# Kernel tuning notes

Hardware: AMD Instinct MI355X
Metric: run time of the kernel (lower is better)

The kernel has to match this reference:

```python
import jax, jax.numpy as jnp
import numpy as np

B, L, DIN, W, H, NL = 4, 1024, 768, 12288, 8, 2
BOTTLENECK = 64
DB = W // BOTTLENECK        # 192: total bottlenecked attention dim
HD = DB // H                # 24: per-head dim
K = 32                      # topk
LAM = 1.0 / (4 * DIN)
EPS = 1e-6


def setup_inputs() -> dict:
    key = jax.random.key(0)
    ks = jax.random.split(key, 8)
    x_input = jax.random.normal(ks[0], (B, L, DIN), jnp.float32)
    # decoder dictionary (torch: randn; scaled for numeric stability)
    D = jax.random.normal(ks[1], (W, DIN), jnp.float32) * 0.02
    b = jnp.zeros((1, DIN), jnp.float32)
    # per-attn-layer bottlenecked projections, stacked over layers
    Wq = jax.random.normal(ks[2], (NL, W, DB), jnp.float32) * 0.02
    Wk = jax.random.normal(ks[3], (NL, W, DB), jnp.float32) * 0.02
    Wv = jax.random.normal(ks[4], (NL, W, DB), jnp.float32) * 0.02
    Wo = jax.random.normal(ks[5], (NL, DB, W), jnp.float32) * 0.02
    bq = jnp.zeros((NL, DB), jnp.float32)
    bk = jnp.zeros((NL, DB), jnp.float32)
    bv = jnp.zeros((NL, DB), jnp.float32)
    bo = jnp.zeros((NL, W), jnp.float32)
    return {"x_input": x_input, "D": D, "b": b, "Wq": Wq, "bq": bq,
            "Wk": Wk, "bk": bk, "Wv": Wv, "bv": bv, "Wo": Wo, "bo": bo}


def _attention(z_ctx, z_in, Wq, bq, Wk, bk, Wv, bv, Wo, bo):
    # queries from current codes, keys/values from shifted context codes
    q = (z_in @ Wq + bq).reshape(B, L, H, HD)
    k = (z_ctx @ Wk + bk).reshape(B, L, H, HD)
    v = (z_ctx @ Wv + bv).reshape(B, L, H, HD)
    scores = jnp.einsum('bqhd,bkhd->bhqk', q, k) / np.sqrt(HD).astype(np.float32)
    causal = jnp.tril(jnp.ones((L, L), bool))  # query t sees ctx positions <= t
    scores = jnp.where(causal, scores, jnp.float32(-1e30))
    a = jax.nn.softmax(scores, axis=-1)
    o = jnp.einsum('bhqk,bkhd->bqhd', a, v).reshape(B, L, DB)
    return o @ Wo + bo


def reference(x_input, D, b, Wq, bq, Wk, bk, Wv, bv, Wo, bo):
    E = D.T  # tied weights
    x = x_input - b
    z_pred = jnp.zeros((B, L, W), x.dtype)
    for i in range(NL):
        z_in = jax.nn.relu((x * LAM) @ E)                       # [B,L,W]
        z_ctx = jnp.concatenate([jnp.zeros_like(z_in[:, :1]), z_in[:, :-1]], axis=1)
        z_pred_ = jax.nn.relu(_attention(z_ctx, z_in, Wq[i], bq[i], Wk[i], bk[i],
                                         Wv[i], bv[i], Wo[i], bo[i]))
        Dz = z_pred_ @ D                                        # [B,L,DIN]
        Dz_norm = jnp.linalg.norm(Dz, axis=-1, keepdims=True) + EPS
        proj_scale = jnp.sum(Dz * x, axis=-1, keepdims=True) / (Dz_norm ** 2)
        z_pred = z_pred + z_pred_ * proj_scale
        x = x - proj_scale * Dz
    # topk sparsification of the novel codes
    z_novel = jax.nn.relu((x * LAM) @ E)
    zf = z_novel.reshape(-1, W)                                 # [B*L, W]
    _, idx = jax.lax.top_k(zf, K)
    mask = jnp.zeros_like(zf).at[jnp.arange(zf.shape[0])[:, None], idx].set(1.0)
    z_novel = (zf * mask).reshape(B, L, W)
    x_recons = (z_novel + z_pred) @ D + b
    return x_recons
```

## Files before the change

kernel.cpp:

```cpp
#include <hip/hip_runtime.h>
#include <hip/hip_bf16.h>

typedef __attribute__((ext_vector_type(4))) float f32x4;
typedef __attribute__((ext_vector_type(8))) short short8;
typedef __attribute__((ext_vector_type(8))) unsigned short ushort8;
typedef __attribute__((ext_vector_type(4))) unsigned short ushort4v;
typedef __attribute__((ext_vector_type(4))) unsigned int uint4v;

#define DEVFN __device__ __forceinline__

DEVFN float b2f(unsigned short u) { return __uint_as_float(((unsigned)u) << 16); }
DEVFN unsigned short f2b(float f) {
  __hip_bfloat16 h = __float2bfloat16(f);
  return __builtin_bit_cast(unsigned short, h);
}

DEVFN void load_lds16(const void* g, void* l) {
  __builtin_amdgcn_global_load_lds(
      (const __attribute__((address_space(1))) unsigned int*)g,
      (__attribute__((address_space(3))) unsigned int*)l, 16, 0, 0);
}


__global__ void fill_out_zero(float* o, int n) {
  int i = blockIdx.x * 256 + threadIdx.x;
  if (i < n) o[i] = 0.0f;
}

__global__ __launch_bounds__(256) void init_x(
    const float* __restrict__ xin, const float* __restrict__ bvec,
    float* __restrict__ x, unsigned short* __restrict__ xb) {
  size_t i = (size_t)blockIdx.x * 256 + threadIdx.x;
  int col = (int)(i % 768);
  float v = xin[i] - bvec[col];
  x[i] = v;
  xb[i] = f2b(v);
}

__global__ __launch_bounds__(256) void fill_bias(
    float* __restrict__ buf, const float* __restrict__ bias, int ld) {
  size_t i = (size_t)blockIdx.x * 256 + threadIdx.x;
  buf[i] = bias ? bias[(int)(i % ld)] : 0.0f;
}

__global__ __launch_bounds__(256) void conv_f2b(
    const float* __restrict__ in, unsigned short* __restrict__ out) {
  size_t i = ((size_t)blockIdx.x * 256 + threadIdx.x) * 4;
  f32x4 v = *(const f32x4*)(in + i);
  ushort4v w;
#pragma unroll
  for (int e = 0; e < 4; ++e) w[e] = f2b(v[e]);
  *(ushort4v*)(out + i) = w;
}

__global__ __launch_bounds__(256) void transpose_f2b(
    const float* __restrict__ in, unsigned short* __restrict__ out,
    int R, int C) {
  __shared__ float tile[32][33];
  int r0 = blockIdx.x * 32, c0 = blockIdx.y * 32;
  int tx = threadIdx.x & 31, ty = threadIdx.x >> 5;
#pragma unroll
  for (int i = 0; i < 4; ++i)
    tile[ty + i * 8][tx] = in[(size_t)(r0 + ty + i * 8) * C + c0 + tx];
  __syncthreads();
#pragma unroll
  for (int i = 0; i < 4; ++i)
    out[(size_t)(c0 + ty + i * 8) * R + r0 + tx] = f2b(tile[tx][ty + i * 8]);
}

template <int GX, int GY, int GZ, int RX, int RG>
DEVFN void rect_decode(int bid, int& x, int& y, int& z) {
  constexpr int NRG = (GY * GZ) / RG;
  const int xcd = bid & 7;
  const int rr = bid >> 3;
  const int rgx = xcd % NRG, rxx = xcd / NRG;
  const int gl = rr % RG;
  int xl = rr / RG;
  xl = (xl + rgx * (RX / NRG)) % RX;
  const int g = rgx * RG + gl;
  x = rxx * RX + xl;
  y = g % GY;
  z = g / GY;
}

template <typename CT, bool RELU, int SC, bool BIAS, bool SPLITK,
          int GX, int GY, int GZ, int RX, int RG>
__global__ __launch_bounds__(512, 2) void gemm_bt2(
    const unsigned short* __restrict__ A, const unsigned short* __restrict__ B,
    CT* __restrict__ C, const float* __restrict__ bias,
    int K, int ldc, float alpha) {
  __shared__ unsigned short sA[2][256 * 64];
  __shared__ unsigned short sB[2][256 * 64];
  const int tid = threadIdx.x;
  const int wave = tid >> 6, lane = tid & 63;
  int bx, by, bz;
  rect_decode<GX, GY, GZ, RX, RG>((int)blockIdx.x, bx, by, bz);
  const int row0 = bx * 256, col0 = by * 256;
  const unsigned short* Ab = A + (size_t)row0 * K;
  const unsigned short* Bb = B + (size_t)col0 * K;
  const int srow = lane >> 3;
  const int swc = ((lane & 7) ^ srow) * 8;
  const int wm = wave & 1, wn = wave >> 1;
  const int lr = lane & 15;
  const int hi = lane >> 4;
  const int l7 = lane & 7;
  const int ksw0 = (hi ^ l7) * 8;
  const int ksw1 = ((4 + hi) ^ l7) * 8;
  const int klen = SPLITK ? (K / GZ) : K;
  const int kbeg = SPLITK ? bz * klen : 0;
  const int nt = klen / 64;
  f32x4 acc[8][4] = {};
  auto stage = [&](int buf, int t) {
    const int k0 = kbeg + t * 64;
#pragma unroll
    for (int it = 0; it < 8; ++it) {
      int c = wave * 8 + it;
      if (c < 32) {
        int r = c * 8 + srow;
        load_lds16(Ab + (size_t)r * K + k0 + swc, &sA[buf][c * 512]);
      } else {
        int cb = c - 32;
        int r = cb * 8 + srow;
        load_lds16(Bb + (size_t)r * K + k0 + swc, &sB[buf][cb * 512]);
      }
    }
  };
  stage(0, 0);
  for (int t = 0; t < nt; ++t) {
    const int cur = t & 1;
    if (t + 1 < nt) {
      stage(cur ^ 1, t + 1);
      asm volatile("s_waitcnt vmcnt(8)" ::: "memory");
    } else {
      asm volatile("s_waitcnt vmcnt(0)" ::: "memory");
    }
    __builtin_amdgcn_s_barrier();
    asm volatile("" ::: "memory");
    const unsigned short* cA = &sA[cur][0];
    const unsigned short* cB = &sB[cur][0];
#pragma unroll
    for (int ks = 0; ks < 2; ++ks) {
      const int ko = ks ? ksw1 : ksw0;
      short8 af[8], bfr[4];
#pragma unroll
      for (int i = 0; i < 8; ++i)
        af[i] = *(const short8*)&cA[(wm * 128 + i * 16 + lr) * 64 + ko];
#pragma unroll
      for (int j = 0; j < 4; ++j)
        bfr[j] = *(const short8*)&cB[(wn * 64 + j * 16 + lr) * 64 + ko];
#pragma unroll
      for (int i = 0; i < 8; ++i)
#pragma unroll
        for (int j = 0; j < 4; ++j)
          acc[i][j] = __builtin_amdgcn_mfma_f32_16x16x32_bf16(af[i], bfr[j], acc[i][j], 0, 0, 0);
    }
    asm volatile("" ::: "memory");
    __builtin_amdgcn_s_barrier();
  }
  const int rc = (SC == 0) ? 0 : ((row0 >> 10) + 1);
  const int rbase = row0 + rc + wm * 128 + (lane >> 4) * 4;
  const int cbase = col0 + wn * 64 + lr;
#pragma unroll
  for (int j = 0; j < 4; ++j) {
    int col = cbase + j * 16;
    float bv = BIAS ? bias[col] : 0.0f;
#pragma unroll
    for (int i = 0; i < 8; ++i) {
#pragma unroll
      for (int r = 0; r < 4; ++r) {
        float vv = acc[i][j][r] * alpha;
        size_t off = (size_t)(rbase + i * 16 + r) * ldc + col;
        if constexpr (SPLITK) {
          atomicAdd((float*)C + off, vv);
        } else {
          vv += bv;
          if (RELU) vv = fmaxf(vv, 0.0f);
          if constexpr (sizeof(CT) == 2) ((unsigned short*)C)[off] = f2b(vv);
          else C[off] = vv;
        }
      }
    }
  }
}

__global__ __launch_bounds__(256) void gemm_qkv(
    const unsigned short* __restrict__ A, const unsigned short* __restrict__ Bq,
    const float* __restrict__ bq, const float* __restrict__ bk,
    const float* __restrict__ bv,
    float* __restrict__ qb, float* __restrict__ kb, float* __restrict__ vb,
    float* __restrict__ P2) {
  __shared__ unsigned short sA[2][64 * 64];
  __shared__ unsigned short sB[2][192 * 64];
  const int tid = threadIdx.x;
  const int wave = tid >> 6, lane = tid & 63;
  const int bid = (int)blockIdx.x;
  const int xcd = bid & 7;
  const int rr = bid >> 3;
  const int combo = rr % 6;
  const int row = xcd * 8 + rr / 6;
  const int wz = combo >> 1;
  const int s = combo & 1;
  const int shift = (wz > 0);
  const unsigned short* B = Bq + (size_t)wz * 192 * 12288;
  const float* bias = (wz == 0) ? bq : (wz == 1 ? bk : bv);
  float* dst = (s == 0) ? ((wz == 0) ? qb : (wz == 1 ? kb : vb))
                        : (P2 + (size_t)wz * 786432);
  const int row0 = row * 64;
  const int ra = (row0 >> 10) + 1;
  const unsigned short* Ab = A + (size_t)(row0 + ra) * 12288;
  const int srow = lane >> 3;
  const int swc = ((lane & 7) ^ srow) * 8;
  const int wm = wave & 1, wn = wave >> 1;
  const int lr = lane & 15;
  const int hi = lane >> 4;
  const int l7 = lane & 7;
  const int ksw0 = (hi ^ l7) * 8;
  const int ksw1 = ((4 + hi) ^ l7) * 8;
  const int kbeg = s * 6144;
  f32x4 acc[2][6] = {};
  auto stage = [&](int buf, int t) {
    const int k0 = kbeg + t * 64;
#pragma unroll
    for (int it = 0; it < 8; ++it) {
      int c = wave * 8 + it;
      if (c < 8) {
        int r = c * 8 + srow;
        load_lds16(Ab + (size_t)r * 12288 + k0 + swc, &sA[buf][c * 512]);
      } else {
        int cb = c - 8;
        int r = cb * 8 + srow;
        load_lds16(B + (size_t)r * 12288 + k0 + swc, &sB[buf][cb * 512]);
      }
    }
  };
  stage(0, 0);
  for (int t = 0; t < 96; ++t) {
    const int cur = t & 1;
    if (t + 1 < 96) {
      stage(cur ^ 1, t + 1);
      asm volatile("s_waitcnt vmcnt(8)" ::: "memory");
    } else {
      asm volatile("s_waitcnt vmcnt(0)" ::: "memory");
    }
    __builtin_amdgcn_s_barrier();
    asm volatile("" ::: "memory");
    const unsigned short* cA = &sA[cur][0];
    const unsigned short* cB = &sB[cur][0];
#pragma unroll
    for (int ks = 0; ks < 2; ++ks) {
      const int ko = ks ? ksw1 : ksw0;
      short8 af[2], bfr[6];
#pragma unroll
      for (int i = 0; i < 2; ++i)
        af[i] = *(const short8*)&cA[(wm * 32 + i * 16 + lr) * 64 + ko];
#pragma unroll
      for (int j = 0; j < 6; ++j)
        bfr[j] = *(const short8*)&cB[(wn * 96 + j * 16 + lr) * 64 + ko];
#pragma unroll
      for (int i = 0; i < 2; ++i)
#pragma unroll
        for (int j = 0; j < 6; ++j)
          acc[i][j] = __builtin_amdgcn_mfma_f32_16x16x32_bf16(af[i], bfr[j], acc[i][j], 0, 0, 0);
    }
    asm volatile("" ::: "memory");
    __builtin_amdgcn_s_barrier();
  }
  const int rbase = row0 + wm * 32 + (lane >> 4) * 4;
  const int cbase = wn * 96 + lr;
#pragma unroll
  for (int j = 0; j < 6; ++j) {
    int col = cbase + j * 16;
    float bvv = (s == 0) ? bias[col] : 0.0f;
#pragma unroll
    for (int i = 0; i < 2; ++i)
#pragma unroll
      for (int r = 0; r < 4; ++r) {
        int rw = rbase + i * 16 + r;
        if (shift) {
          if ((rw & 1023) == 1023) continue;
          rw += 1;
        }
        dst[(size_t)rw * 192 + col] = acc[i][j][r] + bvv;
      }
  }
}

__global__ __launch_bounds__(256) void qkv_merge(
    const float* __restrict__ P2, float* __restrict__ qb,
    float* __restrict__ kb, float* __restrict__ vb) {
  size_t i = ((size_t)blockIdx.x * 256 + threadIdx.x) * 4;
  const int plane = (int)(i / 786432);
  const size_t o = i - (size_t)plane * 786432;
  float* dst = plane == 0 ? qb : (plane == 1 ? kb : vb);
  f32x4 a = *(const f32x4*)(P2 + i);
  f32x4 b = *(const f32x4*)(dst + o);
#pragma unroll
  for (int e = 0; e < 4; ++e) b[e] += a[e];
  *(f32x4*)(dst + o) = b;
}

__global__ __launch_bounds__(256) void attn_pass1(
    const float* __restrict__ q, const float* __restrict__ k,
    const float* __restrict__ v, float* __restrict__ P) {
  __shared__ float sK[128 * 24];
  __shared__ float sV[128 * 24];
  const int tid = threadIdx.x;
  const int wave = tid >> 6, lane = tid & 63;
  const int xcd = (int)blockIdx.x & 7;
  const int r0 = (int)blockIdx.x >> 3;
  const int bh = xcd * 4 + r0 / 72;
  const int t = r0 % 72;
  const int b = bh >> 3, h = bh & 7;
  int jq = 0;
  while (true) {
    int jn = jq + 1;
    int a2 = jn >> 1;
    int offn = a2 * a2 + a2 + (jn & 1) * (a2 + 1);
    if (jn < 16 && offn <= t) jq = jn; else break;
  }
  const int aq = jq >> 1;
  const int offj = aq * aq + aq + (jq & 1) * (aq + 1);
  const int c = t - offj;
  const int qg = jq * 4 + wave;
  const int qi = lane & 15, ks = lane >> 4;
  const int qpos = qg * 16 + qi;
  const int n = b * 1024 + qpos;
  const int task = bh * 72 + t;
  {
    const float* kg = k + (size_t)(b * 1024 + c * 128) * 192 + h * 24;
    const float* vg = v + (size_t)(b * 1024 + c * 128) * 192 + h * 24;
#pragma unroll
    for (int i = 0; i < 3; ++i) {
      int idx = tid + i * 256;
      int row = idx / 6, seg = idx - row * 6;
      *(f32x4*)&sK[row * 24 + seg * 4] =
          *(const f32x4*)(kg + (size_t)row * 192 + seg * 4);
      *(f32x4*)&sV[row * 24 + seg * 4] =
          *(const f32x4*)(vg + (size_t)row * 192 + seg * 4);
    }
  }
  const float scale = 0.20412414523193154f;
  float qv[24];
  const float* qr = q + (size_t)n * 192 + h * 24;
#pragma unroll
  for (int d = 0; d < 24; ++d) qv[d] = qr[d] * scale;
  __syncthreads();
  float m = -1e30f, l = 0.0f, ov[24] = {};
  const int kb0 = c * 128;
  const int kend = min(qpos, kb0 + 127);
  for (int kp = kb0 + ks; kp <= kend; kp += 4) {
    const f32x4* kr = (const f32x4*)&sK[(kp - kb0) * 24];
    float s0 = 0.0f, s1 = 0.0f, s2 = 0.0f;
#pragma unroll
    for (int j = 0; j < 2; ++j) {
      f32x4 k0 = kr[j * 3 + 0], k1 = kr[j * 3 + 1], k2 = kr[j * 3 + 2];
#pragma unroll
      for (int e = 0; e < 4; ++e) {
        s0 += qv[(j * 3 + 0) * 4 + e] * k0[e];
        s1 += qv[(j * 3 + 1) * 4 + e] * k1[e];
        s2 += qv[(j * 3 + 2) * 4 + e] * k2[e];
      }
    }
    float s = s0 + s1 + s2;
    float mn = fmaxf(m, s);
    float corr = __expf(m - mn);
    float p = __expf(s - mn);
    const f32x4* vr = (const f32x4*)&sV[(kp - kb0) * 24];
    l = l * corr + p;
#pragma unroll
    for (int j = 0; j < 6; ++j) {
      f32x4 vvv = vr[j];
#pragma unroll
      for (int e = 0; e < 4; ++e) ov[j * 4 + e] = ov[j * 4 + e] * corr + p * vvv[e];
    }
    m = mn;
  }
#pragma unroll
  for (int off = 16; off < 64; off <<= 1) {
    float m2 = __shfl_xor(m, off);
    float l2 = __shfl_xor(l, off);
    float mn = fmaxf(m, m2);
    float c1 = __expf(m - mn), c2 = __expf(m2 - mn);
    l = l * c1 + l2 * c2;
#pragma unroll
    for (int d = 0; d < 24; ++d) {
      float o2 = __shfl_xor(ov[d], off);
      ov[d] = ov[d] * c1 + o2 * c2;
    }
    m = mn;
  }
  if (ks == 0) {
    float* pr = P + ((size_t)task * 64 + wave * 16 + qi) * 28;
    pr[0] = m;
    pr[1] = l;
#pragma unroll
    for (int d = 0; d < 24; ++d) pr[2 + d] = ov[d];
  }
}

__global__ __launch_bounds__(192) void attn_merge(
    const float* __restrict__ P, unsigned short* __restrict__ o) {
  const int n = blockIdx.x;
  const int tid = threadIdx.x;
  const int h = tid / 24, d = tid - h * 24;
  const int b = n >> 10, qpos = n & 1023;
  const int qg = qpos >> 4, qi = qpos & 15;
  const int j = qg >> 2, w = qg & 3;
  const int a = j >> 1;
  const int nch = a + 1;
  const int offj = a * a + a + (j & 1) * (a + 1);
  const int bh = b * 8 + h;
  const int base = bh * 72 + offj;
  float M = -1e30f;
  for (int cc = 0; cc < nch; ++cc)
    M = fmaxf(M, P[((size_t)(base + cc) * 64 + w * 16 + qi) * 28]);
  float L = 0.0f, OV = 0.0f;
  for (int cc = 0; cc < nch; ++cc) {
    const float* pr = P + ((size_t)(base + cc) * 64 + w * 16 + qi) * 28;
    float wgt = __expf(pr[0] - M);
    L += pr[1] * wgt;
    OV += pr[2 + d] * wgt;
  }
  o[(size_t)n * 192 + h * 24 + d] = f2b(OV / L);
}

__global__ __launch_bounds__(256) void proj_update(
    const float* __restrict__ Dz, float* __restrict__ x,
    unsigned short* __restrict__ xb) {
  const int n = blockIdx.x;
  const int tid = threadIdx.x;
  const float* dz = Dz + (size_t)n * 768;
  float* xr = x + (size_t)n * 768;
  float dot = 0.0f, s2 = 0.0f;
  for (int i = tid; i < 768; i += 256) {
    float a = dz[i], c = xr[i];
    dot += a * c;
    s2 += a * a;
  }
#pragma unroll
  for (int o2 = 32; o2; o2 >>= 1) {
    dot += __shfl_down(dot, o2);
    s2 += __shfl_down(s2, o2);
  }
  __shared__ float sd[4], ss[4], sp;
  const int wave = tid >> 6, lane = tid & 63;
  if (lane == 0) { sd[wave] = dot; ss[wave] = s2; }
  __syncthreads();
  if (tid == 0) {
    float Dd = sd[0] + sd[1] + sd[2] + sd[3];
    float S = ss[0] + ss[1] + ss[2] + ss[3];
    float nrm = sqrtf(S) + 1e-6f;
    sp = Dd / (nrm * nrm);
  }
  __syncthreads();
  float p = sp;
  for (int i = tid; i < 768; i += 256) {
    float nx = xr[i] - p * dz[i];
    xr[i] = nx;
    xb[(size_t)n * 768 + i] = f2b(nx);
  }
}

DEVFN int sanitize(int v) { return (v & 0x8000) ? 0 : v; }

__global__ __launch_bounds__(256) void topk_rows(
    const unsigned short* __restrict__ zbuf, int* __restrict__ idxo,
    float* __restrict__ valo) {
  const int n = blockIdx.x;
  const int b = n >> 10;
  const int tid = threadIdx.x;
  const int wave = tid >> 6, lane = tid & 63;
  const uint4v* zr = (const uint4v*)(zbuf + (size_t)(n + b + 1) * 12288);
  uint4v pk[6];
#pragma unroll
  for (int j = 0; j < 6; ++j) pk[j] = zr[tid * 6 + j];
  __shared__ int swsum[4];
  __shared__ int seq[256];
  __shared__ int spcnt;
  int lo = 0, hi = 0x7F7F;
  while (lo < hi) {
    int mid = (lo + hi) >> 1;
    int c = 0;
#pragma unroll
    for (int j = 0; j < 6; ++j)
#pragma unroll
      for (int e = 0; e < 4; ++e) {
        unsigned int u = pk[j][e];
        c += (sanitize((int)(u & 0xffffu)) > mid) + (sanitize((int)(u >> 16)) > mid);
      }
#pragma unroll
    for (int o2 = 32; o2; o2 >>= 1) c += __shfl_down(c, o2);
    if (lane == 0) swsum[wave] = c;
    __syncthreads();
    int total = swsum[0] + swsum[1] + swsum[2] + swsum[3];
    __syncthreads();
    if (total < 32) hi = mid; else lo = mid + 1;
  }
  const int T = lo;
  int cgt = 0, ceq = 0;
#pragma unroll
  for (int j = 0; j < 6; ++j)
#pragma unroll
    for (int e = 0; e < 4; ++e) {
      unsigned int u = pk[j][e];
      int v0 = sanitize((int)(u & 0xffffu)), v1 = sanitize((int)(u >> 16));
      cgt += (v0 > T) + (v1 > T);
      ceq += (v0 == T) + (v1 == T);
    }
  int cg = cgt;
#pragma unroll
  for (int o2 = 32; o2; o2 >>= 1) cg += __shfl_down(cg, o2);
  if (lane == 0) swsum[wave] = cg;
  seq[tid] = ceq;
  if (tid == 0) spcnt = 0;
  __syncthreads();
  const int total_gt = swsum[0] + swsum[1] + swsum[2] + swsum[3];
  for (int o2 = 1; o2 < 256; o2 <<= 1) {
    int vv = (tid >= o2) ? seq[tid - o2] : 0;
    __syncthreads();
    seq[tid] += vv;
    __syncthreads();
  }
  const int quota = 32 - total_gt;
  int rank = seq[tid] - ceq;
  int* irow = idxo + (size_t)n * 32;
  float* vrow = valo + (size_t)n * 32;
#pragma unroll
  for (int j = 0; j < 6; ++j)
#pragma unroll
    for (int e = 0; e < 4; ++e) {
      unsigned int u = pk[j][e];
#pragma unroll
      for (int hf = 0; hf < 2; ++hf) {
        int v = sanitize(hf ? (int)(u >> 16) : (int)(u & 0xffffu));
        bool kp = false;
        if (v > T) kp = true;
        else if (v == T) { if (rank < quota) kp = true; ++rank; }
        if (kp) {
          int pos = atomicAdd(&spcnt, 1);
          irow[pos] = tid * 48 + j * 8 + e * 2 + hf;
          vrow[pos] = b2f((unsigned short)v);
        }
      }
    }
}

__global__ __launch_bounds__(256) void sparse_recons(
    const int* __restrict__ idxo, const float* __restrict__ valo,
    const float* __restrict__ x, const float* __restrict__ xin,
    const float* __restrict__ D, float* __restrict__ out) {
  const int n = blockIdx.x;
  const int t = threadIdx.x;
  __shared__ int sidx[32];
  __shared__ float sval[32];
  if (t < 32) { sidx[t] = idxo[(size_t)n * 32 + t]; sval[t] = valo[(size_t)n * 32 + t]; }
  __syncthreads();
  float acc[3];
#pragma unroll
  for (int u = 0; u < 3; ++u) {
    size_t i = (size_t)n * 768 + t + u * 256;
    acc[u] = xin[i] - x[i];
  }
  for (int j = 0; j < 32; ++j) {
    size_t base = (size_t)sidx[j] * 768;
    float vj = sval[j];
#pragma unroll
    for (int u = 0; u < 3; ++u) acc[u] += vj * D[base + t + u * 256];
  }
#pragma unroll
  for (int u = 0; u < 3; ++u) out[(size_t)n * 768 + t + u * 256] = acc[u];
}

extern "C" void kernel_launch(void* const* d_in, const int* in_sizes, int n_in,
                              void* d_out, int out_size, void* d_ws, size_t ws_size,
                              hipStream_t stream) {
  (void)in_sizes; (void)n_in;
  const float* xin  = (const float*)d_in[0];
  const float* D    = (const float*)d_in[1];
  const float* bvec = (const float*)d_in[2];
  const float* Wq   = (const float*)d_in[3];
  const float* bq   = (const float*)d_in[4];
  const float* Wk   = (const float*)d_in[5];
  const float* bk   = (const float*)d_in[6];
  const float* Wv   = (const float*)d_in[7];
  const float* bv   = (const float*)d_in[8];
  const float* Wo   = (const float*)d_in[9];
  const float* bo   = (const float*)d_in[10];
  const float LAM = 1.0f / 3072.0f;

  char* ws = (char*)d_ws;
  size_t off = 0;
  auto alloc = [&](size_t bytes) {
    void* p = ws + off;
    off += (bytes + 255) & ~(size_t)255;
    return p;
  };
  unsigned short* zbuf = (unsigned short*)alloc((size_t)4 * 1025 * 12288 * 2);
  unsigned short* zpred_ = zbuf;
  float* attnP = (float*)zbuf;
  float* x           = (float*)alloc((size_t)4096 * 768 * 4);
  unsigned short* xb = (unsigned short*)alloc((size_t)4096 * 768 * 2);
  float* qb  = (float*)alloc((size_t)4096 * 192 * 4);
  float* kb  = (float*)alloc((size_t)4096 * 192 * 4);
  float* vb  = (float*)alloc((size_t)4096 * 192 * 4);
  unsigned short* ob = (unsigned short*)alloc((size_t)4096 * 192 * 2);
  float* Dz  = (float*)alloc((size_t)4096 * 768 * 4);
  int* idxo  = (int*)alloc((size_t)4096 * 32 * 4);
  float* valo = (float*)alloc((size_t)4096 * 32 * 4);
  const size_t WQKV = (size_t)192 * 12288;
  unsigned short* WqkvT = (unsigned short*)alloc((size_t)6 * WQKV * 2);
  unsigned short* WoT   = (unsigned short*)alloc((size_t)2 * 12288 * 192 * 2);
  unsigned short* Dbt   = (unsigned short*)alloc((size_t)12288 * 768 * 2);
  unsigned short* Dt    = (unsigned short*)alloc((size_t)768 * 12288 * 2);
  const size_t NEED = off;
  float* P2 = Dz;

  if (ws_size < NEED) {
    fill_out_zero<<<(out_size + 255) / 256, 256, 0, stream>>>((float*)d_out, out_size);
    return;
  }

  init_x<<<12288, 256, 0, stream>>>(xin, bvec, x, xb);
  conv_f2b<<<9216, 256, 0, stream>>>(D, Dbt);
  transpose_f2b<<<dim3(384, 24), 256, 0, stream>>>(D, Dt, 12288, 768);
  for (int l = 0; l < 2; ++l) {
    transpose_f2b<<<dim3(384, 6), 256, 0, stream>>>(
        Wq + (size_t)l * 12288 * 192, WqkvT + (size_t)(l * 3 + 0) * WQKV, 12288, 192);
    transpose_f2b<<<dim3(384, 6), 256, 0, stream>>>(
        Wk + (size_t)l * 12288 * 192, WqkvT + (size_t)(l * 3 + 1) * WQKV, 12288, 192);
    transpose_f2b<<<dim3(384, 6), 256, 0, stream>>>(
        Wv + (size_t)l * 12288 * 192, WqkvT + (size_t)(l * 3 + 2) * WQKV, 12288, 192);
    transpose_f2b<<<dim3(6, 384), 256, 0, stream>>>(
        Wo + (size_t)l * 192 * 12288, WoT + (size_t)l * 12288 * 192, 192, 12288);
  }

  for (int l = 0; l < 2; ++l) {
    gemm_bt2<unsigned short, true, 1, false, false, 16, 48, 1, 16, 6>
        <<<768, 512, 0, stream>>>(xb, Dbt, zbuf, nullptr, 768, 12288, LAM);
    fill_bias<<<3072, 256, 0, stream>>>(kb, bk + (size_t)l * 192, 192);
    fill_bias<<<3072, 256, 0, stream>>>(vb, bv + (size_t)l * 192, 192);
    fill_bias<<<9216, 256, 0, stream>>>(P2, nullptr, 192);
    gemm_qkv<<<384, 256, 0, stream>>>(
        zbuf, WqkvT + (size_t)(l * 3) * WQKV,
        bq + (size_t)l * 192, bk + (size_t)l * 192, bv + (size_t)l * 192,
        qb, kb, vb, P2);
    qkv_merge<<<2304, 256, 0, stream>>>(P2, qb, kb, vb);
    attn_pass1<<<2304, 256, 0, stream>>>(qb, kb, vb, attnP);
    attn_merge<<<4096, 192, 0, stream>>>(attnP, ob);
    gemm_bt2<unsigned short, true, 0, true, false, 16, 48, 1, 16, 6>
        <<<768, 512, 0, stream>>>(
        ob, WoT + (size_t)l * 12288 * 192, zpred_, bo + (size_t)l * 12288, 192, 12288, 1.0f);
    fill_bias<<<12288, 256, 0, stream>>>(Dz, nullptr, 768);
    gemm_bt2<float, false, 0, false, true, 16, 3, 4, 8, 3>
        <<<192, 512, 0, stream>>>(zpred_, Dt, Dz, nullptr, 12288, 768, 1.0f);
    proj_update<<<4096, 256, 0, stream>>>(Dz, x, xb);
  }
  gemm_bt2<unsigned short, true, 1, false, false, 16, 48, 1, 16, 6>
      <<<768, 512, 0, stream>>>(xb, Dbt, zbuf, nullptr, 768, 12288, LAM);
  topk_rows<<<4096, 256, 0, stream>>>(zbuf, idxo, valo);
  sparse_recons<<<4096, 256, 0, stream>>>(idxo, valo, x, xin, D, (float*)d_out);
}
```

Measured before the change: 1.266 ms.

## Split GEMM main loop into four sub-phases interleaving staged loads with MFMA

The 256x256 bf16 GEMM mainloop is restructured into four quarter-phases, split by M half and K half. Global-to-LDS loads for A and B halves are issued piecemeal between LDS fragment reads and MFMA blocks, replacing one bulk stage per iteration. An A half is prefetched two iterations ahead into the buffer it has just finished with. This aims to spread memory traffic and hide load latency behind compute, in exchange for more barriers per iteration and more complex buffer-reuse ordering that could race if the waitcnt and barrier placement is wrong.

```diff
diff --git a/kernel.cpp b/kernel.cpp
--- a/kernel.cpp
+++ b/kernel.cpp
@@ -110,52 +110,110 @@
   const int kbeg = SPLITK ? bz * klen : 0;
   const int nt = klen / 64;
   f32x4 acc[8][4] = {};
-  auto stage = [&](int buf, int t) {
-    const int k0 = kbeg + t * 64;
-#pragma unroll
-    for (int it = 0; it < 8; ++it) {
-      int c = wave * 8 + it;
-      if (c < 32) {
-        int r = c * 8 + srow;
-        load_lds16(Ab + (size_t)r * K + k0 + swc, &sA[buf][c * 512]);
-      } else {
-        int cb = c - 32;
-        int r = cb * 8 + srow;
-        load_lds16(Bb + (size_t)r * K + k0 + swc, &sB[buf][cb * 512]);
-      }
+  auto stageA = [&](int buf, int tt, int mh) {
+    const int k0 = kbeg + tt * 64;
+#pragma unroll
+    for (int it = 0; it < 2; ++it) {
+      int idx = wave * 2 + it;
+      int c = mh * 8 + (idx & 7) + ((idx & 8) ? 16 : 0);
+      int r = c * 8 + srow;
+      load_lds16(Ab + (size_t)r * K + k0 + swc, &sA[buf][c * 512]);
     }
   };
-  stage(0, 0);
+  auto stageB = [&](int buf, int tt, int h) {
+    const int k0 = kbeg + tt * 64;
+#pragma unroll
+    for (int it = 0; it < 2; ++it) {
+      int idx = wave * 2 + it;
+      int cb = h * 16 + idx;
+      int r = cb * 8 + srow;
+      load_lds16(Bb + (size_t)r * K + k0 + swc, &sB[buf][cb * 512]);
+    }
+  };
+  stageA(0, 0, 0); stageB(0, 0, 0); stageA(0, 0, 1); stageB(0, 0, 1);
+  if (nt > 1) stageA(1, 1, 0);
+  asm volatile("s_waitcnt vmcnt(2)" ::: "memory");
+  __builtin_amdgcn_s_barrier();
+  asm volatile("" ::: "memory");
   for (int t = 0; t < nt; ++t) {
-    const int cur = t & 1;
-    if (t + 1 < nt) {
-      stage(cur ^ 1, t + 1);
-      asm volatile("s_waitcnt vmcnt(8)" ::: "memory");
+    const int cur = t & 1, nxt = cur ^ 1;
+    const unsigned short* cA = &sA[cur][0];
+    const unsigned short* cB = &sB[cur][0];
+    {
+      short8 af[4], bfr[4];
+#pragma unroll
+      for (int i = 0; i < 4; ++i)
+        af[i] = *(const short8*)&cA[(wm * 128 + i * 16 + lr) * 64 + ksw0];
+#pragma unroll
+      for (int j = 0; j < 4; ++j)
+        bfr[j] = *(const short8*)&cB[(wn * 64 + j * 16 + lr) * 64 + ksw0];
+      if (t + 1 < nt) { stageA(nxt, t + 1, 1); stageB(nxt, t + 1, 0); }
+#pragma unroll
+      for (int i = 0; i < 4; ++i)
+#pragma unroll
+        for (int j = 0; j < 4; ++j)
+          acc[i][j] = __builtin_amdgcn_mfma_f32_16x16x32_bf16(af[i], bfr[j], acc[i][j], 0, 0, 0);
+    }
+    asm volatile("" ::: "memory");
+    __builtin_amdgcn_s_barrier();
+    asm volatile("" ::: "memory");
+    {
+      short8 af[4], bfr[4];
+#pragma unroll
+      for (int i = 0; i < 4; ++i)
+        af[i] = *(const short8*)&cA[(wm * 128 + i * 16 + lr) * 64 + ksw1];
+#pragma unroll
+      for (int j = 0; j < 4; ++j)
+        bfr[j] = *(const short8*)&cB[(wn * 64 + j * 16 + lr) * 64 + ksw1];
+      if (t + 1 < nt) stageB(nxt, t + 1, 1);
+#pragma unroll
+      for (int i = 0; i < 4; ++i)
+#pragma unroll
+        for (int j = 0; j < 4; ++j)
+          acc[i][j] = __builtin_amdgcn_mfma_f32_16x16x32_bf16(af[i], bfr[j], acc[i][j], 0, 0, 0);
+    }
+    asm volatile("" ::: "memory");
+    __builtin_amdgcn_s_barrier();
+    asm volatile("" ::: "memory");
+    {
+      short8 af[4], bfr[4];
+#pragma unroll
+      for (int i = 0; i < 4; ++i)
+        af[i] = *(const short8*)&cA[(wm * 128 + 64 + i * 16 + lr) * 64 + ksw0];
+#pragma unroll
+      for (int j = 0; j < 4; ++j)
+        bfr[j] = *(const short8*)&cB[(wn * 64 + j * 16 + lr) * 64 + ksw0];
+      if (t + 2 < nt) stageA(cur, t + 2, 0);
+#pragma unroll
+      for (int i = 0; i < 4; ++i)
+#pragma unroll
+        for (int j = 0; j < 4; ++j)
+          acc[4 + i][j] = __builtin_amdgcn_mfma_f32_16x16x32_bf16(af[i], bfr[j], acc[4 + i][j], 0, 0, 0);
+    }
+    asm volatile("" ::: "memory");
+    __builtin_amdgcn_s_barrier();
+    asm volatile("" ::: "memory");
+    {
+      short8 af[4], bfr[4];
+#pragma unroll
+      for (int i = 0; i < 4; ++i)
+        af[i] = *(const short8*)&cA[(wm * 128 + 64 + i * 16 + lr) * 64 + ksw1];
+#pragma unroll
+      for (int j = 0; j < 4; ++j)
+        bfr[j] = *(const short8*)&cB[(wn * 64 + j * 16 + lr) * 64 + ksw1];
+#pragma unroll
+      for (int i = 0; i < 4; ++i)
+#pragma unroll
+        for (int j = 0; j < 4; ++j)
+          acc[4 + i][j] = __builtin_amdgcn_mfma_f32_16x16x32_bf16(af[i], bfr[j], acc[4 + i][j], 0, 0, 0);
+    }
+    if (t + 2 < nt) {
+      asm volatile("s_waitcnt vmcnt(2)" ::: "memory");
     } else {
       asm volatile("s_waitcnt vmcnt(0)" ::: "memory");
     }
     __builtin_amdgcn_s_barrier();
     asm volatile("" ::: "memory");
-    const unsigned short* cA = &sA[cur][0];
-    const unsigned short* cB = &sB[cur][0];
-#pragma unroll
-    for (int ks = 0; ks < 2; ++ks) {
-      const int ko = ks ? ksw1 : ksw0;
-      short8 af[8], bfr[4];
-#pragma unroll
-      for (int i = 0; i < 8; ++i)
-        af[i] = *(const short8*)&cA[(wm * 128 + i * 16 + lr) * 64 + ko];
-#pragma unroll
-      for (int j = 0; j < 4; ++j)
-        bfr[j] = *(const short8*)&cB[(wn * 64 + j * 16 + lr) * 64 + ko];
-#pragma unroll
-      for (int i = 0; i < 8; ++i)
-#pragma unroll
-        for (int j = 0; j < 4; ++j)
-          acc[i][j] = __builtin_amdgcn_mfma_f32_16x16x32_bf16(af[i], bfr[j], acc[i][j], 0, 0, 0);
-    }
-    asm volatile("" ::: "memory");
-    __builtin_amdgcn_s_barrier();
   }
   const int rc = (SC == 0) ? 0 : ((row0 >> 10) + 1);
   const int rbase = row0 + rc + wm * 128 + (lane >> 4) * 4;
```

Measured after the change: 1.317 ms. 1.04x slower.
